# Performance work log

Measured on AMD Instinct MI355X. Metric: run time of the kernel, lower is better.

The kernel has to match this reference:

```python
import math
import jax, jax.numpy as jnp
import numpy as np
from jax import lax

MUL = 16          # multiplicity of 0e and 1o in irreps_in/out
NB = 4            # num_radial_basis
DIAM = 5.0        # kernel diameter (mm)
R = DIAM / 2.0
STEP_MM = 1.0     # isotropic voxel step


def _lattice_constants():
    """Constant lattice, spherical harmonics (component norm) and radial embedding."""
    s = int(math.floor(R / STEP_MM))                       # 2 -> side 5
    c = np.arange(-s, s + 1.0) * STEP_MM
    lat = np.stack(np.meshgrid(c, c, c, indexing='ij'), axis=-1)   # [5,5,5,3]
    norm = np.linalg.norm(lat, axis=-1)                    # [5,5,5]
    safe = np.where(norm == 0.0, 1.0, norm)
    nvec = np.where(norm[..., None] > 0.0, lat / safe[..., None], 0.0)
    sh1 = np.sqrt(3.0) * nvec                              # l=1 SH, component norm; 0 at origin
    # soft_one_hot_linspace, basis='smooth_finite', start_zero=end_zero=True
    values = np.linspace(0.0, R, NB + 2)[1:-1]             # [NB]
    step = R / (NB + 1)
    d = (norm[..., None] - values) / step                  # [5,5,5,NB]
    dd = np.clip(d, -1.0 + 1e-9, 1.0 - 1e-9)
    emb = np.where(np.abs(d) < 1.0,
                   1.14136 * np.e ** 2 * np.exp(-1.0 / (1.0 - dd ** 2)), 0.0)
    nlat = float(lat.shape[0] * lat.shape[1] * lat.shape[2])
    return (jnp.asarray(sh1, jnp.float32), jnp.asarray(emb, jnp.float32), nlat)

_SH1, _EMB, _NLAT = _lattice_constants()


def _build_kernel(w000, w011, w101, w110, sc0, sc1):
    """Radial basis x Clebsch-Gordan kernel build. Returns [5,5,5,64,64] (XYZIO)."""
    # per-path spatially varying radial weights [x,y,z,u,w]
    r000 = jnp.einsum('xyzb,buw->xyzuw', _EMB, w000) / _NLAT
    r011 = jnp.einsum('xyzb,buw->xyzuw', _EMB, w011) / _NLAT
    r101 = jnp.einsum('xyzb,buw->xyzuw', _EMB, w101) / _NLAT
    r110 = jnp.einsum('xyzb,buw->xyzuw', _EMB, w110) / _NLAT
    X, Y, Z = _EMB.shape[:3]
    eye3 = jnp.eye(3, dtype=w000.dtype)
    # CG (orthonormal per output component):
    # 0e x 0e -> 0e : C = 1
    k00 = r000                                                        # [...,16,16]
    # 0e x 1o -> 1o : C[j,k] = delta
    k01 = jnp.einsum('xyzuw,xyzk->xyzuwk', r011, _SH1).reshape(X, Y, Z, MUL, 3 * MUL)
    # 1o x 0e -> 1o : C[i,k] = delta (sh0 component = 1 everywhere)
    k11 = jnp.einsum('xyzuw,ik->xyzuiwk', r101, eye3).reshape(X, Y, Z, 3 * MUL, 3 * MUL)
    # 1o x 1o -> 0e : C[i,j] = delta/sqrt(3)
    k10 = jnp.einsum('xyzuw,xyzi->xyzuiw', r110, _SH1).reshape(X, Y, Z, 3 * MUL, MUL) / jnp.sqrt(3.0)
    top = jnp.concatenate([k00, k01], axis=-1)   # [...,16,64]
    bot = jnp.concatenate([k10, k11], axis=-1)   # [...,48,64]
    k = jnp.concatenate([top, bot], axis=-2)     # [...,64,64]
    # self-connection overwrites the center tap (FunctionalLinear, std 1/sqrt(mul))
    lin00 = sc0 / jnp.sqrt(float(MUL))
    lin11 = jnp.einsum('uw,ik->uiwk', sc1 / jnp.sqrt(float(MUL)), eye3).reshape(3 * MUL, 3 * MUL)
    z16 = jnp.zeros((MUL, 3 * MUL), dtype=w000.dtype)
    lin = jnp.concatenate([
        jnp.concatenate([lin00, z16], axis=1),
        jnp.concatenate([z16.T, lin11], axis=1)], axis=0)             # [64,64]
    k = k.at[X // 2, Y // 2, Z // 2].set(lin)
    return k


def setup_inputs() -> dict:
    key = jax.random.key(0)
    ks = jax.random.split(key, 7)
    std_tp = 1.0 / math.sqrt(2 * MUL)   # fan-in: 2 paths x mul=16 per output irrep
    std_sc = 1.0 / math.sqrt(MUL)
    return {
        'x': jax.random.normal(ks[0], (2, 48, 48, 48, 4 * MUL), jnp.float32),
        'w000': std_tp * jax.random.normal(ks[1], (NB, MUL, MUL), jnp.float32),
        'w011': std_tp * jax.random.normal(ks[2], (NB, MUL, MUL), jnp.float32),
        'w101': std_tp * jax.random.normal(ks[3], (NB, MUL, MUL), jnp.float32),
        'w110': std_tp * jax.random.normal(ks[4], (NB, MUL, MUL), jnp.float32),
        'sc0': std_sc * jax.random.normal(ks[5], (MUL, MUL), jnp.float32),
        'sc1': std_sc * jax.random.normal(ks[6], (MUL, MUL), jnp.float32),
    }


def reference(x, w000, w011, w101, w110, sc0, sc1):
    k = _build_kernel(w000, w011, w101, w110, sc0, sc1)
    return lax.conv_general_dilated(
        lhs=x, rhs=k, window_strides=(1, 1, 1), padding='SAME',
        dimension_numbers=('NXYZC', 'XYZIO', 'NXYZC'))
```

## Files before the change

kernel.cpp:

```cpp
#include <hip/hip_runtime.h>
#include <math.h>

typedef __attribute__((ext_vector_type(8))) short short8;
typedef __attribute__((ext_vector_type(4))) float float4v;

#define NS 48
#define PS 52
#define NC 64

__device__ __align__(16) unsigned short g_xb[(size_t)2 * PS * PS * PS * NC];
__device__ __align__(16) unsigned short g_kb[125 * 2 * 4 * 64 * 8];

__device__ __forceinline__ unsigned short bf16r(float f) {
  unsigned u = __builtin_bit_cast(unsigned, f);
  u = (u + 0x7FFFu + ((u >> 16) & 1u)) >> 16;
  return (unsigned short)u;
}

__global__ __launch_bounds__(256) void pad_cast(const float* __restrict__ x) {
  const int bx = blockIdx.x;
  const int n = blockIdx.y;
  const int xx = bx / 52, yy = bx % 52;
  const bool inxy = (xx >= 2) && (xx < 50) && (yy >= 2) && (yy < 50);
  unsigned short* dst = g_xb + (((size_t)n * 52 + xx) * 52 + yy) * 3328;
  const float* src = x + ((((size_t)n * 48 + (xx - 2)) * 48 + (yy - 2)) * 48) * 64;
#pragma unroll 1
  for (int tt = threadIdx.x; tt < 832; tt += 256) {
    const int zz = tt >> 4;
    const int i4 = (tt & 15) * 4;
    ushort4 v = make_ushort4(0, 0, 0, 0);
    if (inxy && zz >= 2 && zz < 50) {
      const float4 f = *(const float4*)(src + (size_t)(zz - 2) * 64 + i4);
      v.x = bf16r(f.x); v.y = bf16r(f.y); v.z = bf16r(f.z); v.w = bf16r(f.w);
    }
    *(ushort4*)(dst + (size_t)zz * 64 + i4) = v;
  }
}

__global__ __launch_bounds__(256) void build_kb(
    const float* __restrict__ w000, const float* __restrict__ w011,
    const float* __restrict__ w101, const float* __restrict__ w110,
    const float* __restrict__ sc0,  const float* __restrict__ sc1) {
  const int tap = blockIdx.x;
  const int tz = tap % 5, ty = (tap / 5) % 5, tx = tap / 25;
  const float cx = (float)(tx - 2), cy = (float)(ty - 2), cz = (float)(tz - 2);
  const float norm = sqrtf(cx * cx + cy * cy + cz * cz);
  const float inv = (norm > 0.f) ? (1.f / norm) : 0.f;
  const float SQ3 = 1.7320508075688772f;
  const float sh[3] = {SQ3 * cx * inv, SQ3 * cy * inv, SQ3 * cz * inv};
  float emb[4];
#pragma unroll
  for (int b = 0; b < 4; ++b) {
    const float v = 0.5f * (float)(b + 1);
    const float d = (norm - v) * 2.0f;
    emb[b] = (fabsf(d) < 1.f) ? 1.14136f * expf(2.f - 1.f / (1.f - d * d)) : 0.f;
  }
  const bool center = (tap == 62);
  const float INV_NLAT = 1.0f / 125.0f;
  const float INV_SQ3 = 0.57735026918962576f;
  for (int e = threadIdx.x; e < 4096; e += blockDim.x) {
    const int r = e >> 6, c = e & 63;
    float val = 0.f;
    if (center) {
      if (r < 16 && c < 16) {
        val = sc0[r * 16 + c] * 0.25f;
      } else if (r >= 16 && c >= 16) {
        const int u = (r - 16) / 3, i = (r - 16) % 3;
        const int w = (c - 16) / 3, kc = (c - 16) % 3;
        val = (i == kc) ? sc1[u * 16 + w] * 0.25f : 0.f;
      }
    } else {
      if (r < 16 && c < 16) {
        float a = 0.f;
#pragma unroll
        for (int b = 0; b < 4; ++b) a += emb[b] * w000[(b * 16 + r) * 16 + c];
        val = a * INV_NLAT;
      } else if (r < 16) {
        const int w = (c - 16) / 3, kc = (c - 16) % 3;
        float a = 0.f;
#pragma unroll
        for (int b = 0; b < 4; ++b) a += emb[b] * w011[(b * 16 + r) * 16 + w];
        val = a * INV_NLAT * sh[kc];
      } else if (c < 16) {
        const int u = (r - 16) / 3, i = (r - 16) % 3;
        float a = 0.f;
#pragma unroll
        for (int b = 0; b < 4; ++b) a += emb[b] * w110[(b * 16 + u) * 16 + c];
        val = a * INV_NLAT * sh[i] * INV_SQ3;
      } else {
        const int u = (r - 16) / 3, i = (r - 16) % 3;
        const int w = (c - 16) / 3, kc = (c - 16) % 3;
        if (i == kc) {
          float a = 0.f;
#pragma unroll
          for (int b = 0; b < 4; ++b) a += emb[b] * w101[(b * 16 + u) * 16 + w];
          val = a * INV_NLAT;
        }
      }
    }
    const int ik = r >> 5;
    const int lane = ((r >> 3) & 3) * 16 + (c & 15);
    const int of = c >> 4;
    const int j = r & 7;
    g_kb[((size_t)((tap * 2 + ik) * 4 + of) * 64 + lane) * 8 + j] = bf16r(val);
  }
}

__global__ __launch_bounds__(256, 5) void conv_mfma(float* __restrict__ out) {
  __shared__ __align__(16) char xs[8 * 52 * 64];
  const int t = threadIdx.x;
  const int l = t & 63;
  const int wid = t >> 6;
  const int m = l & 15;
  const int kq = l >> 4;
  const int bid = blockIdx.x;
  const int wg = (bid & 7) * 144 + (bid >> 3);
  const int X = wg % 48;
  const int yg = (wg / 48) % 12;
  const int n = wg / 576;
  const int y0 = yg << 2;

  float4v acc[3][4];
  const float4v zero4 = {0.f, 0.f, 0.f, 0.f};
#pragma unroll
  for (int zt = 0; zt < 3; ++zt)
#pragma unroll
    for (int of = 0; of < 4; ++of) acc[zt][of] = zero4;

#pragma unroll 1
  for (int dx = 0; dx < 5; ++dx) {
    const unsigned short* gx =
        g_xb + ((size_t)n * PS + (X + dx)) * 173056 + (size_t)y0 * 3328;
#pragma unroll 1
    for (int h = 0; h < 2; ++h) {
      __syncthreads();
#pragma unroll
      for (int s = 0; s < 7; ++s) {
        const int cl = t + (s << 8);
        if (cl < 1664) {
          const int row = cl >> 2, p = cl & 3;
          const int jy = row / 52, zz = row - jy * 52;
          const int sc = p ^ (zz & 3);
          const unsigned short* g = gx + jy * 3328 + zz * 64 + h * 32 + sc * 8;
          char* ldsd = xs + (size_t)((t >> 6) * 64 + (s << 8)) * 16;
          __builtin_amdgcn_global_load_lds(
              (const __attribute__((address_space(1))) unsigned*)g,
              (__attribute__((address_space(3))) unsigned*)ldsd, 16, 0, 0);
        }
      }
      __syncthreads();

#pragma unroll 1
      for (int dy = 0; dy < 5; ++dy) {
        const int rb0 = (wid + dy) * 52 + m;
        const int tapb = ((dx * 5 + dy) * 5) * 2 + h;
#pragma unroll
        for (int dz = 0; dz < 5; ++dz) {
          const unsigned short* kbp =
              g_kb + (size_t)(tapb + dz * 2) * 2048 + l * 8;
          const short8 b0 = *(const short8*)(kbp);
          const short8 b1 = *(const short8*)(kbp + 512);
          const short8 b2 = *(const short8*)(kbp + 1024);
          const short8 b3 = *(const short8*)(kbp + 1536);
          short8 a[3];
#pragma unroll
          for (int zt = 0; zt < 3; ++zt) {
            const int row = rb0 + zt * 16 + dz;
            const int byte = row * 64 + ((kq ^ (row & 3)) << 4);
            a[zt] = *(const short8*)(xs + byte);
          }
#pragma unroll
          for (int zt = 0; zt < 3; ++zt) {
            acc[zt][0] = __builtin_amdgcn_mfma_f32_16x16x32_bf16(a[zt], b0, acc[zt][0], 0, 0, 0);
            acc[zt][1] = __builtin_amdgcn_mfma_f32_16x16x32_bf16(a[zt], b1, acc[zt][1], 0, 0, 0);
            acc[zt][2] = __builtin_amdgcn_mfma_f32_16x16x32_bf16(a[zt], b2, acc[zt][2], 0, 0, 0);
            acc[zt][3] = __builtin_amdgcn_mfma_f32_16x16x32_bf16(a[zt], b3, acc[zt][3], 0, 0, 0);
          }
        }
      }
    }
  }

  float* op = out + ((((size_t)n * NS + X) * NS + (y0 + wid)) * NS) * NC;
#pragma unroll
  for (int zt = 0; zt < 3; ++zt) {
#pragma unroll
    for (int of = 0; of < 4; ++of) {
#pragma unroll
      for (int r = 0; r < 4; ++r) {
        const int z = zt * 16 + kq * 4 + r;
        const int o = of * 16 + m;
        op[(size_t)z * NC + o] = acc[zt][of][r];
      }
    }
  }
}

extern "C" void kernel_launch(void* const* d_in, const int* in_sizes, int n_in,
                              void* d_out, int out_size, void* d_ws, size_t ws_size,
                              hipStream_t stream) {
  const float* x    = (const float*)d_in[0];
  const float* w000 = (const float*)d_in[1];
  const float* w011 = (const float*)d_in[2];
  const float* w101 = (const float*)d_in[3];
  const float* w110 = (const float*)d_in[4];
  const float* sc0  = (const float*)d_in[5];
  const float* sc1  = (const float*)d_in[6];
  float* out = (float*)d_out;

  pad_cast<<<dim3(52 * 52, 2), 256, 0, stream>>>(x);
  build_kb<<<125, 256, 0, stream>>>(w000, w011, w101, w110, sc0, sc1);
  conv_mfma<<<1152, 256, 0, stream>>>(out);
}
```

Baseline: 290.4 us.

## Give each wave two y rows so kernel B-fragments are reused across more output

Each wave now computes two output y rows instead of one, so a workgroup covers 8 y rows and the grid halves to 576 blocks. Each B-fragment loaded from the global kernel buffer is reused by 24 MFMAs instead of 12, which cuts global kernel-weight traffic per output. The LDS tile grows to 12 rows, and the swizzle is changed to use (row>>1)&3 to avoid bank conflicts. In exchange, accumulator registers double and occupancy drops to 3 blocks per CU, and the smaller grid may not fill all CUs evenly.

```diff
diff --git a/kernel.cpp b/kernel.cpp
--- a/kernel.cpp
+++ b/kernel.cpp
@@ -106,26 +106,28 @@
   }
 }
 
-__global__ __launch_bounds__(256, 5) void conv_mfma(float* __restrict__ out) {
-  __shared__ __align__(16) char xs[8 * 52 * 64];
+__global__ __launch_bounds__(256, 3) void conv_mfma(float* __restrict__ out) {
+  __shared__ __align__(16) char xs[12 * 52 * 64];
   const int t = threadIdx.x;
   const int l = t & 63;
   const int wid = t >> 6;
   const int m = l & 15;
   const int kq = l >> 4;
   const int bid = blockIdx.x;
-  const int wg = (bid & 7) * 144 + (bid >> 3);
+  const int wg = (bid & 7) * 72 + (bid >> 3);
   const int X = wg % 48;
-  const int yg = (wg / 48) % 12;
-  const int n = wg / 576;
-  const int y0 = yg << 2;
-
-  float4v acc[3][4];
+  const int yg = (wg / 48) % 6;
+  const int n = wg / 288;
+  const int y0 = yg << 3;
+
+  float4v acc[2][3][4];
   const float4v zero4 = {0.f, 0.f, 0.f, 0.f};
 #pragma unroll
-  for (int zt = 0; zt < 3; ++zt)
-#pragma unroll
-    for (int of = 0; of < 4; ++of) acc[zt][of] = zero4;
+  for (int y = 0; y < 2; ++y)
+#pragma unroll
+    for (int zt = 0; zt < 3; ++zt)
+#pragma unroll
+      for (int of = 0; of < 4; ++of) acc[y][zt][of] = zero4;
 
 #pragma unroll 1
   for (int dx = 0; dx < 5; ++dx) {
@@ -135,12 +137,12 @@
     for (int h = 0; h < 2; ++h) {
       __syncthreads();
 #pragma unroll
-      for (int s = 0; s < 7; ++s) {
+      for (int s = 0; s < 10; ++s) {
         const int cl = t + (s << 8);
-        if (cl < 1664) {
-          const int row = cl >> 2, p = cl & 3;
-          const int jy = row / 52, zz = row - jy * 52;
-          const int sc = p ^ (zz & 3);
+        if (cl < 2496) {
+          const int ry = cl >> 2, p = cl & 3;
+          const int jy = ry / 52, zz = ry - jy * 52;
+          const int sc = p ^ ((ry >> 1) & 3);
           const unsigned short* g = gx + jy * 3328 + zz * 64 + h * 32 + sc * 8;
           char* ldsd = xs + (size_t)((t >> 6) * 64 + (s << 8)) * 16;
           __builtin_amdgcn_global_load_lds(
@@ -152,7 +154,7 @@
 
 #pragma unroll 1
       for (int dy = 0; dy < 5; ++dy) {
-        const int rb0 = (wid + dy) * 52 + m;
+        const int rbase = (2 * wid + dy) * 52 + m;
         const int tapb = ((dx * 5 + dy) * 5) * 2 + h;
 #pragma unroll
         for (int dz = 0; dz < 5; ++dz) {
@@ -162,35 +164,45 @@
           const short8 b1 = *(const short8*)(kbp + 512);
           const short8 b2 = *(const short8*)(kbp + 1024);
           const short8 b3 = *(const short8*)(kbp + 1536);
-          short8 a[3];
-#pragma unroll
-          for (int zt = 0; zt < 3; ++zt) {
-            const int row = rb0 + zt * 16 + dz;
-            const int byte = row * 64 + ((kq ^ (row & 3)) << 4);
-            a[zt] = *(const short8*)(xs + byte);
+          short8 a[2][3];
+#pragma unroll
+          for (int y = 0; y < 2; ++y) {
+#pragma unroll
+            for (int zt = 0; zt < 3; ++zt) {
+              const int ry = rbase + y * 52 + zt * 16 + dz;
+              const int byte = ry * 64 + ((kq ^ ((ry >> 1) & 3)) << 4);
+              a[y][zt] = *(const short8*)(xs + byte);
+            }
           }
 #pragma unroll
-          for (int zt = 0; zt < 3; ++zt) {
-            acc[zt][0] = __builtin_amdgcn_mfma_f32_16x16x32_bf16(a[zt], b0, acc[zt][0], 0, 0, 0);
-            acc[zt][1] = __builtin_amdgcn_mfma_f32_16x16x32_bf16(a[zt], b1, acc[zt][1], 0, 0, 0);
-            acc[zt][2] = __builtin_amdgcn_mfma_f32_16x16x32_bf16(a[zt], b2, acc[zt][2], 0, 0, 0);
-            acc[zt][3] = __builtin_amdgcn_mfma_f32_16x16x32_bf16(a[zt], b3, acc[zt][3], 0, 0, 0);
+          for (int y = 0; y < 2; ++y) {
+#pragma unroll
+            for (int zt = 0; zt < 3; ++zt) {
+              acc[y][zt][0] = __builtin_amdgcn_mfma_f32_16x16x32_bf16(a[y][zt], b0, acc[y][zt][0], 0, 0, 0);
+              acc[y][zt][1] = __builtin_amdgcn_mfma_f32_16x16x32_bf16(a[y][zt], b1, acc[y][zt][1], 0, 0, 0);
+              acc[y][zt][2] = __builtin_amdgcn_mfma_f32_16x16x32_bf16(a[y][zt], b2, acc[y][zt][2], 0, 0, 0);
+              acc[y][zt][3] = __builtin_amdgcn_mfma_f32_16x16x32_bf16(a[y][zt], b3, acc[y][zt][3], 0, 0, 0);
+            }
           }
         }
       }
     }
   }
 
-  float* op = out + ((((size_t)n * NS + X) * NS + (y0 + wid)) * NS) * NC;
-#pragma unroll
-  for (int zt = 0; zt < 3; ++zt) {
-#pragma unroll
-    for (int of = 0; of < 4; ++of) {
-#pragma unroll
-      for (int r = 0; r < 4; ++r) {
-        const int z = zt * 16 + kq * 4 + r;
-        const int o = of * 16 + m;
-        op[(size_t)z * NC + o] = acc[zt][of][r];
+#pragma unroll
+  for (int y = 0; y < 2; ++y) {
+    float* op = out +
+        ((((size_t)n * NS + X) * NS + (y0 + 2 * wid + y)) * NS) * NC;
+#pragma unroll
+    for (int zt = 0; zt < 3; ++zt) {
+#pragma unroll
+      for (int of = 0; of < 4; ++of) {
+#pragma unroll
+        for (int r = 0; r < 4; ++r) {
+          const int z = zt * 16 + kq * 4 + r;
+          const int o = of * 16 + m;
+          op[(size_t)z * NC + o] = acc[y][zt][of][r];
+        }
       }
     }
   }
@@ -210,5 +222,5 @@
 
   pad_cast<<<dim3(52 * 52, 2), 256, 0, stream>>>(x);
   build_kb<<<125, 256, 0, stream>>>(w000, w011, w101, w110, sc0, sc1);
-  conv_mfma<<<1152, 256, 0, stream>>>(out);
-}
+  conv_mfma<<<576, 256, 0, stream>>>(out);
+}
```

Measured after the change: 251.3 us. 13.5% less time.
